# Performance work log

Measured on AMD Instinct MI355X. Metric: run time of the kernel, lower is better.

Reference implementation:

```python
import jax, jax.numpy as jnp
import numpy as np

N, M, D = 6144, 6144, 128
EPS = 1e-12


def setup_inputs() -> dict:
    key = jax.random.key(0)
    k1, k2 = jax.random.split(key)
    desc1 = jax.random.normal(k1, (N, D), dtype=jnp.float32)
    desc2 = jax.random.normal(k2, (M, D), dtype=jnp.float32)
    # DISK descriptors are unit-normalized; distances in the docstring are in [0, 2]
    desc1 = desc1 / jnp.linalg.norm(desc1, axis=-1, keepdims=True)
    desc2 = desc2 / jnp.linalg.norm(desc2, axis=-1, keepdims=True)
    inverse_T = jnp.asarray(15.0, dtype=jnp.float32)  # learned scalar nn.Parameter
    return {"desc1": desc1, "desc2": desc2, "inverse_T": inverse_T}


def reference(desc1, desc2, inverse_T):
    # pairwise Euclidean distance matrix [N, M]
    sq1 = jnp.sum(desc1 * desc1, axis=-1)            # [N]
    sq2 = jnp.sum(desc2 * desc2, axis=-1)            # [M]
    inner = desc1 @ desc2.T                           # [N, M] GEMM, D=128
    d2 = sq1[:, None] + sq2[None, :] - 2.0 * inner
    distances = jnp.sqrt(jnp.maximum(d2, 0.0) + EPS)  # [N, M]

    affinity = -inverse_T * distances                 # scaled logits

    # Categorical(logits=affinity).logits  == log_softmax over rows
    # Categorical(logits=affinity.T).logits.T == log_softmax over columns
    logp_I = jax.nn.log_softmax(affinity, axis=1)     # row distribution [N, M]
    logp_T = jax.nn.log_softmax(affinity, axis=0)     # col distribution [N, M]

    dense_logp = logp_I + logp_T                      # dual-softmax log prob
    dense_p = jnp.exp(logp_I) * jnp.exp(logp_T)       # dual-softmax prob

    # mle(): argmax matches with cycle-consistency check
    maxes_I = jnp.argmax(affinity, axis=1)            # [N] best col per row
    maxes_T = jnp.argmax(affinity, axis=0)            # [M] best row per col
    idx = jnp.arange(N)
    cycle_consistent = maxes_T[maxes_I] == idx        # [N] bool mask
    # Original returns stack([right[paired_left], paired_left]) over the
    # consistent subset; here we keep fixed shape [2, N] + the mask
    # (matches[:, i] valid iff cycle_consistent[i]).
    matches = jnp.stack([idx, maxes_I], axis=0)       # [2, N] int

    return dense_logp, dense_p, matches, cycle_consistent
```

## Files before the change

### kernel.cpp

```cpp
#include <hip/hip_runtime.h>
#include <hip/hip_bf16.h>
#include <stdint.h>

#define NROWS 6144
#define MCOLS 6144
#define DDIM  128
#define EPSQ  1e-12f
#define NTC   48

typedef unsigned long long ull;
typedef __attribute__((ext_vector_type(8))) short short8;
typedef __attribute__((ext_vector_type(4))) float floatx4;

__device__ __forceinline__ ull makeKey(float v, int idx) {
    unsigned u = __float_as_uint(v);
    u = (u & 0x80000000u) ? ~u : (u | 0x80000000u);
    return ((ull)u << 32) | (ull)(0xFFFFFFFFu - (unsigned)idx);
}
__device__ __forceinline__ int decodeKeyIdx(ull k) {
    return (int)(0xFFFFFFFFu - (unsigned)(k & 0xFFFFFFFFull));
}
__device__ __forceinline__ unsigned short f2bf(float f) {
    unsigned u = __float_as_uint(f);
    u += 0x7fffu + ((u >> 16) & 1);
    return (unsigned short)(u >> 16);
}

#define DPPF(x, ctrl) __uint_as_float(__builtin_amdgcn_update_dpp( \
    0, (int)__float_as_uint(x), (ctrl), 0xF, 0xF, false))
#define DPPI(x, ctrl) __builtin_amdgcn_update_dpp(0, (x), (ctrl), 0xF, 0xF, false)
#define ROR8 0x128
#define ROR4 0x124
#define ROR2 0x122
#define ROR1 0x121

#define GLOAD16(g, l) \
  __builtin_amdgcn_global_load_lds((const __attribute__((address_space(1))) unsigned int*)(g), \
                                   (__attribute__((address_space(3))) unsigned int*)(l), 16, 0, 0)

__device__ __forceinline__ void tileCoord(int& rowBase, int& colBase) {
    int id  = blockIdx.x;
    int wid = (id & 7) * (NTC * NTC / 8) + (id >> 3);
    rowBase = (wid / NTC) * 128;
    colBase = (wid % NTC) * 128;
}

__global__ __launch_bounds__(256) void convert_kernel(
    const float* __restrict__ d1, const float* __restrict__ d2,
    unsigned short* __restrict__ s1, unsigned short* __restrict__ s2,
    float* __restrict__ sq1, float* __restrict__ sq2,
    unsigned* __restrict__ zero_region)
{
    int tid = blockIdx.x * 256 + threadIdx.x;
    if (tid < 36864) zero_region[tid] = 0u;

    int gw = tid >> 6;
    int lane = threadIdx.x & 63;
    if (gw >= NROWS + MCOLS) return;
    bool isA = gw < NROWS;
    int row = isA ? gw : gw - NROWS;
    const float* src = (isA ? d1 : d2) + (size_t)row * DDIM;
    unsigned short* dst = (isA ? s1 : s2) + (size_t)row * 256;

    float2 v = *(const float2*)(src + lane * 2);
    float s = v.x * v.x + v.y * v.y;
    #pragma unroll
    for (int m = 1; m < 64; m <<= 1) s += __shfl_xor(s, m, 64);
    if (lane == 0) { if (isA) sq1[row] = s; else sq2[row] = s; }

    unsigned short h0 = f2bf(v.x), h1 = f2bf(v.y);
    float r0 = v.x - __uint_as_float((unsigned)h0 << 16);
    float r1 = v.y - __uint_as_float((unsigned)h1 << 16);
    unsigned short l0 = f2bf(r0), l1 = f2bf(r1);
    int c  = lane >> 5;
    int e  = (2 * lane) & 63;
    int pe = e ^ ((row & 7) << 3);
    *(unsigned*)(dst + c * 128 + pe)      = (unsigned)h0 | ((unsigned)h1 << 16);
    *(unsigned*)(dst + c * 128 + 64 + pe) = (unsigned)l0 | ((unsigned)l1 << 16);
}

__device__ __forceinline__ void stageBuf(
    const unsigned short* __restrict__ gpanel, unsigned short* buf,
    int c, int h, int t)
{
    #pragma unroll
    for (int it = 0; it < 2; ++it) {
        int li = t * 8 + it * 4096;
        int r  = li >> 6, e = li & 63;
        int gi = r * 256 + c * 128 + h * 64 + e;
        GLOAD16(gpanel + gi, &buf[li]);
    }
}

__device__ __forceinline__ void computeSplit(
    const unsigned short* Ab_, const unsigned short* Bb_,
    int lane, int wr, int wc, floatx4 acc[4][2])
{
    const int l15 = lane & 15;
    const int q16 = (lane >> 4) * 16;
    const int sw  = (l15 & 7) << 4;
    const char* Ab = (const char*)Ab_;
    const char* Bb = (const char*)Bb_;
    #pragma unroll
    for (int ks = 0; ks < 2; ++ks) {
        const int kk = (ks * 64 + q16) ^ sw;
        short8 af[4], bf[2];
        #pragma unroll
        for (int mi = 0; mi < 4; ++mi)
            af[mi] = *(const short8*)(Ab + (wr * 64 + mi * 16 + l15) * 128 + kk);
        #pragma unroll
        for (int ni = 0; ni < 2; ++ni)
            bf[ni] = *(const short8*)(Bb + (wc * 32 + ni * 16 + l15) * 128 + kk);
        #pragma unroll
        for (int mi = 0; mi < 4; ++mi)
            #pragma unroll
            for (int ni = 0; ni < 2; ++ni)
                acc[mi][ni] = __builtin_amdgcn_mfma_f32_16x16x32_bf16(
                    bf[ni], af[mi], acc[mi][ni], 0, 0, 0);
    }
}

__global__ __launch_bounds__(512, 4) void gemm_reduce_kernel(
    const unsigned short* __restrict__ s1, const unsigned short* __restrict__ s2,
    const float* __restrict__ invT,
    const float* __restrict__ sq1, const float* __restrict__ sq2,
    float* __restrict__ rowsum, float* __restrict__ colsum,
    ull* __restrict__ rowkey, ull* __restrict__ colkey)
{
    __shared__ unsigned short A0[8192], A1[8192], B0[8192], B1[8192];
    __shared__ float lRowS[128], lColS[128];
    __shared__ ull   lRowK[128], lColK[128];

    const int t = threadIdx.x;
    const int lane = t & 63;
    const int wave = t >> 6;
    const int wr = wave >> 2, wc = wave & 3;
    int rowBase, colBase;
    tileCoord(rowBase, colBase);
    const unsigned short* gA = s1 + (size_t)rowBase * 256;
    const unsigned short* gB = s2 + (size_t)colBase * 256;

    if (t < 128) { lRowS[t] = 0.f; lColS[t] = 0.f; lRowK[t] = 0ull; lColK[t] = 0ull; }

    floatx4 acc[4][2] = {};
    stageBuf(gA, A0, 0, 0, t); stageBuf(gB, B0, 0, 0, t);
    __syncthreads();
    stageBuf(gA, A1, 0, 1, t); stageBuf(gB, B1, 0, 1, t);
    computeSplit(A0, B0, lane, wr, wc, acc);
    __syncthreads();
    computeSplit(A0, B1, lane, wr, wc, acc);
    __syncthreads();
    stageBuf(gA, A0, 1, 0, t); stageBuf(gB, B1, 1, 0, t);
    computeSplit(A1, B0, lane, wr, wc, acc);
    __syncthreads();
    stageBuf(gA, A1, 1, 1, t); stageBuf(gB, B0, 1, 1, t);
    computeSplit(A0, B1, lane, wr, wc, acc);
    __syncthreads();
    computeSplit(A0, B0, lane, wr, wc, acc);
    computeSplit(A1, B1, lane, wr, wc, acc);

    const int l15 = lane & 15;
    const int q   = lane >> 4;
    const float iT = *invT;
    float s1r[4];
    #pragma unroll
    for (int mi = 0; mi < 4; ++mi)
        s1r[mi] = sq1[rowBase + wr * 64 + mi * 16 + l15] + EPSQ;
    const int colLoc0 = wc * 32 + q * 4;
    float4 s2v[2];
    #pragma unroll
    for (int ni = 0; ni < 2; ++ni)
        s2v[ni] = *(const float4*)(sq2 + colBase + colLoc0 + ni * 16);

    float rs[4], rv[4]; int rj[4];
    float cs[2][4], cv[2][4]; int ci[2][4];
    #pragma unroll
    for (int ni = 0; ni < 2; ++ni)
        #pragma unroll
        for (int r = 0; r < 4; ++r) { cs[ni][r] = 0.f; cv[ni][r] = -1e30f; ci[ni][r] = 0; }

    #pragma unroll
    for (int mi = 0; mi < 4; ++mi) {
        const int gi = rowBase + wr * 64 + mi * 16 + l15;
        rs[mi] = 0.f; rv[mi] = -1e30f; rj[mi] = 0;
        #pragma unroll
        for (int ni = 0; ni < 2; ++ni) {
            #pragma unroll
            for (int r = 0; r < 4; ++r) {
                float sv2 = (r == 0) ? s2v[ni].x : (r == 1) ? s2v[ni].y
                          : (r == 2) ? s2v[ni].z : s2v[ni].w;
                float dd = s1r[mi] + sv2 - 2.0f * acc[mi][ni][r];
                float v = -iT * __builtin_amdgcn_sqrtf(fmaxf(dd, EPSQ));
                float e = __expf(v);
                rs[mi] += e;
                if (v > rv[mi]) { rv[mi] = v; rj[mi] = colBase + colLoc0 + ni * 16 + r; }
                cs[ni][r] += e;
                if (v > cv[ni][r]) { cv[ni][r] = v; ci[ni][r] = gi; }
            }
        }
    }

    #pragma unroll
    for (int mi = 0; mi < 4; ++mi) {
        float s = rs[mi];
        s += __shfl_xor(s, 16, 64); s += __shfl_xor(s, 32, 64);
        float v = rv[mi];
        v = fmaxf(v, __shfl_xor(v, 16, 64)); v = fmaxf(v, __shfl_xor(v, 32, 64));
        int cand = (rv[mi] == v) ? rj[mi] : 0x7FFFFFFF;
        cand = min(cand, __shfl_xor(cand, 16, 64));
        cand = min(cand, __shfl_xor(cand, 32, 64));
        if (lane < 16) {
            int idx = wr * 64 + mi * 16 + l15;
            atomicAdd(&lRowS[idx], s);
            atomicMax(&lRowK[idx], makeKey(v, cand));
        }
    }

    #pragma unroll
    for (int ni = 0; ni < 2; ++ni)
        #pragma unroll
        for (int r = 0; r < 4; ++r) {
            float s = cs[ni][r];
            s += DPPF(s, ROR8); s += DPPF(s, ROR4); s += DPPF(s, ROR2); s += DPPF(s, ROR1);
            float v = cv[ni][r];
            v = fmaxf(v, DPPF(v, ROR8)); v = fmaxf(v, DPPF(v, ROR4));
            v = fmaxf(v, DPPF(v, ROR2)); v = fmaxf(v, DPPF(v, ROR1));
            int cand = (cv[ni][r] == v) ? ci[ni][r] : 0x7FFFFFFF;
            cand = min(cand, DPPI(cand, ROR8)); cand = min(cand, DPPI(cand, ROR4));
            cand = min(cand, DPPI(cand, ROR2)); cand = min(cand, DPPI(cand, ROR1));
            if (l15 == 0) {
                int idx = colLoc0 + ni * 16 + r;
                atomicAdd(&lColS[idx], s);
                atomicMax(&lColK[idx], makeKey(v, cand));
            }
        }
    __syncthreads();

    if (t < 128) {
        atomicAdd(&rowsum[rowBase + t], lRowS[t]);
        atomicMax(&rowkey[rowBase + t], lRowK[t]);
    } else if (t < 256) {
        int j = t - 128;
        atomicAdd(&colsum[colBase + j], lColS[j]);
        atomicMax(&colkey[colBase + j], lColK[j]);
    }
}

__global__ __launch_bounds__(256) void finalize_small_kernel(
    const float* __restrict__ rowsum, const ull* __restrict__ rowkey,
    const float* __restrict__ colsum, const ull* __restrict__ colkey,
    float* __restrict__ rowlse, float* __restrict__ collse,
    float* __restrict__ out_matches, float* __restrict__ out_cyc)
{
    int i = blockIdx.x * 256 + threadIdx.x;
    if (i >= NROWS) return;
    rowlse[i] = logf(rowsum[i]);
    collse[i] = logf(colsum[i]);
    int mi = decodeKeyIdx(rowkey[i]);
    out_matches[i]         = (float)i;
    out_matches[NROWS + i] = (float)mi;
    out_cyc[i] = (decodeKeyIdx(colkey[mi]) == i) ? 1.0f : 0.0f;
}

__global__ __launch_bounds__(512, 4) void gemm_write_kernel(
    const unsigned short* __restrict__ s1, const unsigned short* __restrict__ s2,
    const float* __restrict__ invT,
    const float* __restrict__ sq1, const float* __restrict__ sq2,
    const float* __restrict__ rowlse, const float* __restrict__ collse,
    float* __restrict__ logp_out, float* __restrict__ p_out)
{
    __shared__ unsigned short A0[8192], A1[8192], B0[8192], B1[8192];

    const int t = threadIdx.x;
    const int lane = t & 63;
    const int wave = t >> 6;
    const int wr = wave >> 2, wc = wave & 3;
    int rowBase, colBase;
    tileCoord(rowBase, colBase);
    const unsigned short* gA = s1 + (size_t)rowBase * 256;
    const unsigned short* gB = s2 + (size_t)colBase * 256;

    floatx4 acc[4][2] = {};
    stageBuf(gA, A0, 0, 0, t); stageBuf(gB, B0, 0, 0, t);
    __syncthreads();
    stageBuf(gA, A1, 0, 1, t); stageBuf(gB, B1, 1, 0, t);
    computeSplit(A0, B0, lane, wr, wc, acc);
    __syncthreads();
    stageBuf(gA, A0, 1, 0, t);
    computeSplit(A1, B0, lane, wr, wc, acc);
    __syncthreads();
    stageBuf(gA, A1, 1, 1, t);
    computeSplit(A0, B1, lane, wr, wc, acc);
    __syncthreads();
    computeSplit(A1, B1, lane, wr, wc, acc);

    const int l15 = lane & 15;
    const int q   = lane >> 4;
    const float iT = *invT;
    float s1r[4], rl[4];
    #pragma unroll
    for (int mi = 0; mi < 4; ++mi) {
        int gi = rowBase + wr * 64 + mi * 16 + l15;
        s1r[mi] = sq1[gi] + EPSQ;
        rl[mi]  = rowlse[gi];
    }
    const int colLoc0 = wc * 32 + q * 4;
    float4 s2v[2], clv[2];
    #pragma unroll
    for (int ni = 0; ni < 2; ++ni) {
        s2v[ni] = *(const float4*)(sq2    + colBase + colLoc0 + ni * 16);
        clv[ni] = *(const float4*)(collse + colBase + colLoc0 + ni * 16);
    }

    #pragma unroll
    for (int mi = 0; mi < 4; ++mi) {
        const int gi = rowBase + wr * 64 + mi * 16 + l15;
        #pragma unroll
        for (int ni = 0; ni < 2; ++ni) {
            floatx4 ov, pv;
            #pragma unroll
            for (int r = 0; r < 4; ++r) {
                float sv2 = (r == 0) ? s2v[ni].x : (r == 1) ? s2v[ni].y
                          : (r == 2) ? s2v[ni].z : s2v[ni].w;
                float cl  = (r == 0) ? clv[ni].x : (r == 1) ? clv[ni].y
                          : (r == 2) ? clv[ni].z : clv[ni].w;
                float dd = s1r[mi] + sv2 - 2.0f * acc[mi][ni][r];
                float v = -iT * __builtin_amdgcn_sqrtf(fmaxf(dd, EPSQ));
                float o = (v - rl[mi]) + (v - cl);
                ov[r] = o;
                pv[r] = __expf(o);
            }
            size_t off = (size_t)gi * MCOLS + colBase + colLoc0 + ni * 16;
            __builtin_nontemporal_store(ov, (floatx4*)(logp_out + off));
            __builtin_nontemporal_store(pv, (floatx4*)(p_out + off));
        }
    }
}

extern "C" void kernel_launch(void* const* d_in, const int* in_sizes, int n_in,
                              void* d_out, int out_size, void* d_ws, size_t ws_size,
                              hipStream_t stream) {
    const float* d1   = (const float*)d_in[0];
    const float* d2   = (const float*)d_in[1];
    const float* invT = (const float*)d_in[2];

    float* out     = (float*)d_out;
    float* logp    = out;
    float* pout    = out + (size_t)NROWS * MCOLS;
    float* matches = out + 2ull * NROWS * MCOLS;
    float* cyc     = matches + 2 * NROWS;

    char* ws = (char*)d_ws;
    float* rowsum = (float*)(ws + 0);
    float* colsum = (float*)(ws + 24576);
    ull*   rowkey = (ull*)(ws + 49152);
    ull*   colkey = (ull*)(ws + 98304);
    float* sq1    = (float*)(ws + 147456);
    float* sq2    = (float*)(ws + 172032);
    float* rowlse = (float*)(ws + 196608);
    float* collse = (float*)(ws + 221184);
    unsigned short* s1 = (unsigned short*)(ws + 270336);
    unsigned short* s2 = (unsigned short*)(ws + 270336 + 3145728);

    convert_kernel<<<(NROWS + MCOLS) / 4, 256, 0, stream>>>(
        d1, d2, s1, s2, sq1, sq2, (unsigned*)ws);

    gemm_reduce_kernel<<<NTC * NTC, 512, 0, stream>>>(
        s1, s2, invT, sq1, sq2, rowsum, colsum, rowkey, colkey);

    finalize_small_kernel<<<NROWS / 256, 256, 0, stream>>>(
        rowsum, rowkey, colsum, colkey, rowlse, collse, matches, cyc);

    gemm_write_kernel<<<NTC * NTC, 512, 0, stream>>>(
        s1, s2, invT, sq1, sq2, rowlse, collse, logp, pout);
}
```

Measured before the change: 157.2 us.

## Restructure reduce-kernel staging with five LDS buffers and fused dual-B MFMA

```diff
diff --git a/kernel.cpp b/kernel.cpp
--- a/kernel.cpp
+++ b/kernel.cpp
@@ -7,6 +7,7 @@
 #define DDIM  128
 #define EPSQ  1e-12f
 #define NTC   48
+#define LOG2E 1.442695040888963f
 
 typedef unsigned long long ull;
 typedef __attribute__((ext_vector_type(8))) short short8;
@@ -120,6 +121,43 @@
     }
 }
 
+__device__ __forceinline__ void computeSplitAB2(
+    const unsigned short* Ab_, const unsigned short* B0_, const unsigned short* B1_,
+    int lane, int wr, int wc, floatx4 acc[4][2])
+{
+    const int l15 = lane & 15;
+    const int q16 = (lane >> 4) * 16;
+    const int sw  = (l15 & 7) << 4;
+    const char* Ab = (const char*)Ab_;
+    const char* B0 = (const char*)B0_;
+    const char* B1 = (const char*)B1_;
+    #pragma unroll
+    for (int ks = 0; ks < 2; ++ks) {
+        const int kk = (ks * 64 + q16) ^ sw;
+        short8 af[4], bf0[2], bf1[2];
+        #pragma unroll
+        for (int mi = 0; mi < 4; ++mi)
+            af[mi] = *(const short8*)(Ab + (wr * 64 + mi * 16 + l15) * 128 + kk);
+        #pragma unroll
+        for (int ni = 0; ni < 2; ++ni) {
+            bf0[ni] = *(const short8*)(B0 + (wc * 32 + ni * 16 + l15) * 128 + kk);
+            bf1[ni] = *(const short8*)(B1 + (wc * 32 + ni * 16 + l15) * 128 + kk);
+        }
+        #pragma unroll
+        for (int mi = 0; mi < 4; ++mi)
+            #pragma unroll
+            for (int ni = 0; ni < 2; ++ni)
+                acc[mi][ni] = __builtin_amdgcn_mfma_f32_16x16x32_bf16(
+                    bf0[ni], af[mi], acc[mi][ni], 0, 0, 0);
+        #pragma unroll
+        for (int mi = 0; mi < 4; ++mi)
+            #pragma unroll
+            for (int ni = 0; ni < 2; ++ni)
+                acc[mi][ni] = __builtin_amdgcn_mfma_f32_16x16x32_bf16(
+                    bf1[ni], af[mi], acc[mi][ni], 0, 0, 0);
+    }
+}
+
 __global__ __launch_bounds__(512, 4) void gemm_reduce_kernel(
     const unsigned short* __restrict__ s1, const unsigned short* __restrict__ s2,
     const float* __restrict__ invT,
@@ -127,41 +165,47 @@
     float* __restrict__ rowsum, float* __restrict__ colsum,
     ull* __restrict__ rowkey, ull* __restrict__ colkey)
 {
-    __shared__ unsigned short A0[8192], A1[8192], B0[8192], B1[8192];
-    __shared__ float lRowS[128], lColS[128];
-    __shared__ ull   lRowK[128], lColK[128];
+    __shared__ unsigned short P[8192], Q[8192], R[8192], S[8192], T[8192];
+    float* lRowS = (float*)R;
+    float* lColS = (float*)((char*)R + 512);
+    ull*   lRowK = (ull*)((char*)R + 1024);
+    ull*   lColK = (ull*)((char*)R + 2048);
 
     const int t = threadIdx.x;
     const int lane = t & 63;
-    const int wave = t >> 6;
-    const int wr = wave >> 2, wc = wave & 3;
+    const int wr = (t >> 6) >> 2, wc = (t >> 6) & 3;
     int rowBase, colBase;
     tileCoord(rowBase, colBase);
     const unsigned short* gA = s1 + (size_t)rowBase * 256;
     const unsigned short* gB = s2 + (size_t)colBase * 256;
 
+    floatx4 acc[4][2] = {};
+    stageBuf(gA, P, 0, 0, t); stageBuf(gB, Q, 0, 0, t);
+    stageBuf(gA, R, 0, 1, t); stageBuf(gB, S, 0, 1, t);
+    __syncthreads();
+    stageBuf(gA, T, 1, 0, t);
+    __builtin_amdgcn_s_setprio(1);
+    computeSplitAB2(P, Q, S, lane, wr, wc, acc);
+    __builtin_amdgcn_s_setprio(0);
+    __syncthreads();
+    stageBuf(gB, P, 1, 0, t); stageBuf(gB, S, 1, 1, t);
+    __builtin_amdgcn_s_setprio(1);
+    computeSplit(R, Q, lane, wr, wc, acc);
+    __builtin_amdgcn_s_setprio(0);
+    __syncthreads();
+    stageBuf(gA, Q, 1, 1, t);
     if (t < 128) { lRowS[t] = 0.f; lColS[t] = 0.f; lRowK[t] = 0ull; lColK[t] = 0ull; }
-
-    floatx4 acc[4][2] = {};
-    stageBuf(gA, A0, 0, 0, t); stageBuf(gB, B0, 0, 0, t);
-    __syncthreads();
-    stageBuf(gA, A1, 0, 1, t); stageBuf(gB, B1, 0, 1, t);
-    computeSplit(A0, B0, lane, wr, wc, acc);
-    __syncthreads();
-    computeSplit(A0, B1, lane, wr, wc, acc);
-    __syncthreads();
-    stageBuf(gA, A0, 1, 0, t); stageBuf(gB, B1, 1, 0, t);
-    computeSplit(A1, B0, lane, wr, wc, acc);
-    __syncthreads();
-    stageBuf(gA, A1, 1, 1, t); stageBuf(gB, B0, 1, 1, t);
-    computeSplit(A0, B1, lane, wr, wc, acc);
-    __syncthreads();
-    computeSplit(A0, B0, lane, wr, wc, acc);
-    computeSplit(A1, B1, lane, wr, wc, acc);
+    __builtin_amdgcn_s_setprio(1);
+    computeSplitAB2(T, P, S, lane, wr, wc, acc);
+    __builtin_amdgcn_s_setprio(0);
+    __syncthreads();
+    __builtin_amdgcn_s_setprio(1);
+    computeSplit(Q, P, lane, wr, wc, acc);
+    __builtin_amdgcn_s_setprio(0);
 
     const int l15 = lane & 15;
     const int q   = lane >> 4;
-    const float iT = *invT;
+    const float iT2 = (*invT) * LOG2E;
     float s1r[4];
     #pragma unroll
     for (int mi = 0; mi < 4; ++mi)
@@ -190,8 +234,8 @@
                 float sv2 = (r == 0) ? s2v[ni].x : (r == 1) ? s2v[ni].y
                           : (r == 2) ? s2v[ni].z : s2v[ni].w;
                 float dd = s1r[mi] + sv2 - 2.0f * acc[mi][ni][r];
-                float v = -iT * __builtin_amdgcn_sqrtf(fmaxf(dd, EPSQ));
-                float e = __expf(v);
+                float v = -iT2 * __builtin_amdgcn_sqrtf(fmaxf(dd, EPSQ));
+                float e = __builtin_amdgcn_exp2f(v);
                 rs[mi] += e;
                 if (v > rv[mi]) { rv[mi] = v; rj[mi] = colBase + colLoc0 + ni * 16 + r; }
                 cs[ni][r] += e;
@@ -273,8 +317,7 @@
 
     const int t = threadIdx.x;
     const int lane = t & 63;
-    const int wave = t >> 6;
-    const int wr = wave >> 2, wc = wave & 3;
+    const int wr = (t >> 6) >> 2, wc = (t >> 6) & 3;
     int rowBase, colBase;
     tileCoord(rowBase, colBase);
     const unsigned short* gA = s1 + (size_t)rowBase * 256;
@@ -284,15 +327,23 @@
     stageBuf(gA, A0, 0, 0, t); stageBuf(gB, B0, 0, 0, t);
     __syncthreads();
     stageBuf(gA, A1, 0, 1, t); stageBuf(gB, B1, 1, 0, t);
+    __builtin_amdgcn_s_setprio(1);
     computeSplit(A0, B0, lane, wr, wc, acc);
+    __builtin_amdgcn_s_setprio(0);
     __syncthreads();
     stageBuf(gA, A0, 1, 0, t);
+    __builtin_amdgcn_s_setprio(1);
     computeSplit(A1, B0, lane, wr, wc, acc);
+    __builtin_amdgcn_s_setprio(0);
     __syncthreads();
     stageBuf(gA, A1, 1, 1, t);
+    __builtin_amdgcn_s_setprio(1);
     computeSplit(A0, B1, lane, wr, wc, acc);
-    __syncthreads();
+    __builtin_amdgcn_s_setprio(0);
+    __syncthreads();
+    __builtin_amdgcn_s_setprio(1);
     computeSplit(A1, B1, lane, wr, wc, acc);
+    __builtin_amdgcn_s_setprio(0);
 
     const int l15 = lane & 15;
     const int q   = lane >> 4;
```

Measured after the change: 159.4 us. Within noise of the previous version (+1.4%).
